# Kernel tuning notes

Hardware: AMD Instinct MI355X
Metric: run time of the kernel (lower is better)

## Reference

```python
import jax, jax.numpy as jnp
import numpy as np

HEADS = 4
KD = 32          # key_dim per head
LEVELS = 2
G = 3            # 2**dims - 1 HP orientation groups
STRENGTH = 0.25
DECAY = 0.6
LN_EPS = 1e-5
MIX_EPS = 1e-3


def _layernorm(x, g, b):
    m = jnp.mean(x, axis=-1, keepdims=True)
    v = jnp.var(x, axis=-1, keepdims=True)
    return (x - m) * jax.lax.rsqrt(v + LN_EPS) * g + b


def _dwt2(x):
    # Haar analysis, periodic/even sizes. [B,H,W,C] -> [B,H/2,W/2,4C] (LL,LH,HL,HH)
    x00 = x[:, 0::2, 0::2]; x01 = x[:, 0::2, 1::2]
    x10 = x[:, 1::2, 0::2]; x11 = x[:, 1::2, 1::2]
    ll = (x00 + x01 + x10 + x11) * 0.5
    lh = (x00 - x01 + x10 - x11) * 0.5
    hl = (x00 + x01 - x10 - x11) * 0.5
    hh = (x00 - x01 - x10 + x11) * 0.5
    return jnp.concatenate([ll, lh, hl, hh], axis=-1)


def _idwt2(w):
    # exact Haar synthesis: [B,H/2,W/2,4C] -> [B,H,W,C]
    ll, lh, hl, hh = jnp.split(w, 4, axis=-1)
    x00 = (ll + lh + hl + hh) * 0.5
    x01 = (ll - lh + hl - hh) * 0.5
    x10 = (ll + lh - hl - hh) * 0.5
    x11 = (ll - lh - hl + hh) * 0.5
    B, H2, W2, C = ll.shape
    r0 = jnp.stack([x00, x01], axis=3).reshape(B, H2, 2 * W2, C)  # interleave W
    r1 = jnp.stack([x10, x11], axis=3).reshape(B, H2, 2 * W2, C)
    return jnp.stack([r0, r1], axis=2).reshape(B, 2 * H2, 2 * W2, C)  # interleave H


def _axial_mhsa(x, p):
    # AxialMHSAND: sequential sweep over spatial axes; each pass is
    # proj(attn(softmax(QK^T/sqrt(d)) V)) on norm(x), qkv via 1x1 conv (=matmul).
    g, b, wq, bq, wk, bk, wv, bv, wp, bp = p
    scale = KD ** -0.5
    for axis in (1, 2):
        X = _layernorm(x, g, b)
        B, H, W, _ = X.shape
        Q = (X @ wq + bq).reshape(B, H, W, HEADS, KD)
        K = (X @ wk + bk).reshape(B, H, W, HEADS, KD)
        V = (X @ wv + bv).reshape(B, H, W, HEADS, KD)
        if axis == 1:  # attend along H, batch over (B, W, heads)
            A = jax.nn.softmax(jnp.einsum('bqwnd,bkwnd->bwnqk', Q, K) * scale, axis=-1)
            Y = jnp.einsum('bwnqk,bkwnd->bqwnd', A, V)
        else:          # attend along W, batch over (B, H, heads)
            A = jax.nn.softmax(jnp.einsum('bhqnd,bhknd->bhnqk', Q, K) * scale, axis=-1)
            Y = jnp.einsum('bhnqk,bhknd->bhqnd', A, V)
        x = Y.reshape(B, H, W, HEADS * KD) @ wp + bp
    return x


def setup_inputs() -> dict:
    key = jax.random.key(0)
    ks = jax.random.split(key, 24)
    C = 64
    HD = HEADS * KD
    s = 0.02
    inp = {'x': jax.random.normal(ks[0], (4, 256, 256, C), jnp.float32)}
    i = 1
    for pre in ('lp', 'hp'):
        inp[pre + '_ln_g'] = jnp.ones((C,), jnp.float32)
        inp[pre + '_ln_b'] = jnp.zeros((C,), jnp.float32)
        inp[pre + '_wq'] = jax.random.normal(ks[i], (C, HD), jnp.float32) * s
        inp[pre + '_bq'] = jax.random.normal(ks[i + 1], (HD,), jnp.float32) * s
        inp[pre + '_wk'] = jax.random.normal(ks[i + 2], (C, HD), jnp.float32) * s
        inp[pre + '_bk'] = jax.random.normal(ks[i + 3], (HD,), jnp.float32) * s
        inp[pre + '_wv'] = jax.random.normal(ks[i + 4], (C, HD), jnp.float32) * s
        inp[pre + '_bv'] = jax.random.normal(ks[i + 5], (HD,), jnp.float32) * s
        inp[pre + '_wp'] = jax.random.normal(ks[i + 6], (HD, C), jnp.float32) * s
        inp[pre + '_bp'] = jax.random.normal(ks[i + 7], (C,), jnp.float32) * s
        i += 8
    mix = jnp.eye(G, dtype=jnp.float32) + MIX_EPS * (jnp.ones((G, G), jnp.float32) - jnp.eye(G, dtype=jnp.float32))
    inp['mix_w0'] = mix
    inp['mix_w1'] = mix
    return inp


def reference(x, lp_ln_g, lp_ln_b, lp_wq, lp_bq, lp_wk, lp_bk, lp_wv, lp_bv, lp_wp, lp_bp,
              hp_ln_g, hp_ln_b, hp_wq, hp_bq, hp_wk, hp_bk, hp_wv, hp_bv, hp_wp, hp_bp,
              mix_w0, mix_w1):
    lp_p = (lp_ln_g, lp_ln_b, lp_wq, lp_bq, lp_wk, lp_bk, lp_wv, lp_bv, lp_wp, lp_bp)
    hp_p = (hp_ln_g, hp_ln_b, hp_wq, hp_bq, hp_wk, hp_bk, hp_wv, hp_bv, hp_wp, hp_bp)
    mix_ws = [mix_w0, mix_w1]
    C = x.shape[-1]
    cur = x
    hps = []
    for _ in range(LEVELS):  # analysis pyramid
        w = _dwt2(cur)
        hps.append(w[..., C:])
        cur = w[..., :C]
    # deepest LP: axial attention, residual with full strength
    cur = cur + STRENGTH * _axial_mhsa(cur, lp_p)
    for l in reversed(range(LEVELS)):  # synthesis with per-level HP processing
        hp = hps[l]
        B, H2, W2, _ = hp.shape
        gain = STRENGTH * (DECAY ** (LEVELS - 1 - l))  # coarser levels stronger
        hp_g = hp.reshape(B, H2, W2, G, C)
        mixed = jnp.einsum('gd,bhwdc->bhwgc', mix_ws[l], hp_g)  # OrientationMix
        batched = mixed.transpose(3, 0, 1, 2, 4).reshape(G * B, H2, W2, C)
        att = _axial_mhsa(batched, hp_p)  # shared hp_attn across groups/levels
        att = att.reshape(G, B, H2, W2, C).transpose(1, 2, 3, 0, 4).reshape(B, H2, W2, G * C)
        hp_out = hp + gain * att
        cur = _idwt2(jnp.concatenate([cur, hp_out], axis=-1))
    return cur
```

## Files before the change

kernel.cpp:

```cpp
#include <hip/hip_runtime.h>

#define LN_EPS 1e-5f
#define QSCALE 0.25500526578425445f

typedef __attribute__((ext_vector_type(8))) short bf16x8;
typedef __attribute__((ext_vector_type(4))) float f32x4;

#define MFMA16(A, B, C) __builtin_amdgcn_mfma_f32_16x16x32_bf16(A, B, C, 0, 0, 0)

static __device__ __forceinline__ unsigned short f2bf_rne(float f) {
    union { unsigned int i; float f; } c; c.f = f;
    unsigned int i = c.i;
    return (unsigned short)((i + 0x7fffu + ((i >> 16) & 1u)) >> 16);
}
static __device__ __forceinline__ void bfstore2(unsigned short* p, float x, float y) {
    *(unsigned int*)p = (unsigned int)f2bf_rne(x) | ((unsigned int)f2bf_rne(y) << 16);
}
static __device__ __forceinline__ unsigned pk2(float a, float b) {
    return __builtin_amdgcn_perm(__builtin_bit_cast(unsigned, b),
                                 __builtin_bit_cast(unsigned, a), 0x07060302u);
}
static __device__ __forceinline__ unsigned short tb16(float f) {
    return (unsigned short)(__builtin_bit_cast(unsigned, f) >> 16);
}
static __device__ __forceinline__ float bftrunc(float f) {
    return __builtin_bit_cast(float, __builtin_bit_cast(unsigned, f) & 0xFFFF0000u);
}

__global__ void dwt_kernel(const float4* __restrict__ in, float4* __restrict__ ll,
                           float4* __restrict__ hp, int B, int H2, int W2) {
    const int i = blockIdx.x * blockDim.x + threadIdx.x;
    const int total = B * H2 * W2 * 16;
    if (i >= total) return;
    const int c4 = i & 15;
    int t = i >> 4;
    const int w2 = t % W2; t /= W2;
    const int h2 = t % H2;
    const int b = t / H2;
    const int W = W2 * 2;
    const size_t base = (((size_t)b * (H2 * 2) + 2 * h2) * W + 2 * w2) * 16 + c4;
    const float4 x00 = in[base];
    const float4 x01 = in[base + 16];
    const float4 x10 = in[base + (size_t)W * 16];
    const float4 x11 = in[base + (size_t)W * 16 + 16];
    float4 vll, vlh, vhl, vhh;
#define DWTC(a) \
    vll.a = (x00.a + x01.a + x10.a + x11.a) * 0.5f; \
    vlh.a = (x00.a - x01.a + x10.a - x11.a) * 0.5f; \
    vhl.a = (x00.a + x01.a - x10.a - x11.a) * 0.5f; \
    vhh.a = (x00.a - x01.a - x10.a + x11.a) * 0.5f;
    DWTC(x) DWTC(y) DWTC(z) DWTC(w)
#undef DWTC
    const size_t oi = ((size_t)b * H2 + h2) * W2 + w2;
    ll[oi * 16 + c4] = vll;
    hp[oi * 48 + c4] = vlh;
    hp[oi * 48 + 16 + c4] = vhl;
    hp[oi * 48 + 32 + c4] = vhh;
}

__global__ void idwt_kernel(const float4* __restrict__ cur, const float4* __restrict__ hp,
                            const float4* __restrict__ att, float gain,
                            float4* __restrict__ out, int B, int H2, int W2) {
    const int i = blockIdx.x * blockDim.x + threadIdx.x;
    const int total = B * H2 * W2 * 16;
    if (i >= total) return;
    const int c4 = i & 15;
    int t = i >> 4;
    const int w2 = t % W2; t /= W2;
    const int h2 = t % H2;
    const int b = t / H2;
    const size_t oi = ((size_t)b * H2 + h2) * W2 + w2;
    const size_t sp = (size_t)h2 * W2 + w2;
    const size_t gstr = (size_t)B * H2 * W2;
    const float4 vll = cur[oi * 16 + c4];
    float4 vlh = hp[oi * 48 + c4];
    float4 vhl = hp[oi * 48 + 16 + c4];
    float4 vhh = hp[oi * 48 + 32 + c4];
    const float4 a0 = att[((size_t)b * H2 * W2 + sp) * 16 + c4];
    const float4 a1 = att[((size_t)b * H2 * W2 + gstr + sp) * 16 + c4];
    const float4 a2 = att[((size_t)b * H2 * W2 + 2 * gstr + sp) * 16 + c4];
#define ADDG(a) \
    vlh.a = fmaf(gain, a0.a, vlh.a); \
    vhl.a = fmaf(gain, a1.a, vhl.a); \
    vhh.a = fmaf(gain, a2.a, vhh.a);
    ADDG(x) ADDG(y) ADDG(z) ADDG(w)
#undef ADDG
    float4 x00, x01, x10, x11;
#define IDWTC(a) \
    x00.a = (vll.a + vlh.a + vhl.a + vhh.a) * 0.5f; \
    x01.a = (vll.a - vlh.a + vhl.a - vhh.a) * 0.5f; \
    x10.a = (vll.a + vlh.a - vhl.a - vhh.a) * 0.5f; \
    x11.a = (vll.a - vlh.a - vhl.a + vhh.a) * 0.5f;
    IDWTC(x) IDWTC(y) IDWTC(z) IDWTC(w)
#undef IDWTC
    const int W = W2 * 2;
    const size_t r0 = (((size_t)b * (H2 * 2) + 2 * h2) * W + 2 * w2) * 16 + c4;
    out[r0] = x00;
    out[r0 + 16] = x01;
    out[r0 + (size_t)W * 16] = x10;
    out[r0 + (size_t)W * 16 + 16] = x11;
}

__global__ void prep_weights(const float* __restrict__ lwq, const float* __restrict__ lwk,
                             const float* __restrict__ lwv, const float* __restrict__ lwp,
                             const float* __restrict__ hwq, const float* __restrict__ hwk,
                             const float* __restrict__ hwv, const float* __restrict__ hwp,
                             unsigned short* __restrict__ wbuf) {
    const int i = blockIdx.x * blockDim.x + threadIdx.x;
    if (i >= 65536) return;
    const int set = i >> 15;
    const int r = i & 32767;
    const float* wq = set ? hwq : lwq;
    const float* wk = set ? hwk : lwk;
    const float* wv = set ? hwv : lwv;
    const float* wp = set ? hwp : lwp;
    float v;
    if (r < 24576) {
        const int nn = r >> 6, c = r & 63;
        const float* w = (nn < 128) ? wq : (nn < 256) ? wk : wv;
        v = w[c * 128 + (nn & 127)];
        if (nn < 128) v *= QSCALE;
    } else {
        const int r2 = r - 24576;
        const int nn = r2 >> 7, d = r2 & 127;
        v = wp[d * 64 + nn];
    }
    wbuf[i] = f2bf_rne(v);
}

struct Job {
    const float* xin;
    const float* mixsrc;
    const float* mixw;
    float* xout;
    const float* basep;
    float res_scale;
    const float* ln_g; const float* ln_b;
    const float* bq; const float* bk; const float* bv; const float* bp;
    const unsigned short* wqkvT;
    const unsigned short* wpT;
};

template<int S>
__global__ __launch_bounds__(512, 4)
void axial_attn(Job jA, Job jB, int nA, int axis)
{
    constexpr int BS = 512;
    constexpr int CK = 32;
    constexpr int NCH = S / CK;
    constexpr int NSI = S / 32;
    constexpr int CSTR = 40;

    __shared__ __align__(16) unsigned short Xs[S * 64];
    __shared__ __align__(16) unsigned short Arena[18432];

    const int tid = threadIdx.x;
    const int lane = tid & 63;
    const int w = tid >> 6;
    const int n16 = lane & 15;
    const int quad = lane >> 4;

    const bool isB = (int)blockIdx.x >= nA;
    const Job j = isB ? jB : jA;
    const int line = isB ? (int)blockIdx.x - nA : (int)blockIdx.x;
    const int lb = line / S;
    const int lr = line - lb * S;
    size_t lbase, tstr;
    if (axis == 1) { lbase = ((size_t)lb * S * S + lr) * 64; tstr = (size_t)S * 64; }
    else           { lbase = ((size_t)lb * S + lr) * (size_t)S * 64; tstr = 64; }

    const float bk = j.bk[w * 16 + n16];
    const float bv = j.bv[w * 16 + n16];

    {
        const int sub = tid & 15;
        const float4 g4 = ((const float4*)j.ln_g)[sub];
        const float4 be4 = ((const float4*)j.ln_b)[sub];
        const float4* x4 = (const float4*)j.xin;
        const float4* hp4 = (const float4*)j.mixsrc;
        const size_t lbase4 = lbase >> 2, tstr4 = tstr >> 2;
        float m0, m1, m2; int bimg;
        if (hp4) {
            const int g = lb >> 2;
            bimg = lb & 3;
            m0 = j.mixw[g * 3 + 0]; m1 = j.mixw[g * 3 + 1]; m2 = j.mixw[g * 3 + 2];
        }
        for (int t = (tid >> 4); t < S; t += BS / 16) {
            float4 v;
            if (hp4) {
                const int pos = (axis == 1) ? (t * S + lr) : (lr * S + t);
                const size_t hb = ((size_t)bimg * S * S + pos) * 48 + sub;
                const float4 h0 = hp4[hb];
                const float4 h1 = hp4[hb + 16];
                const float4 h2 = hp4[hb + 32];
                v.x = m0 * h0.x + m1 * h1.x + m2 * h2.x;
                v.y = m0 * h0.y + m1 * h1.y + m2 * h2.y;
                v.z = m0 * h0.z + m1 * h1.z + m2 * h2.z;
                v.w = m0 * h0.w + m1 * h1.w + m2 * h2.w;
            } else {
                v = x4[lbase4 + (size_t)t * tstr4 + sub];
            }
            float s = v.x + v.y + v.z + v.w;
            float ss = v.x * v.x + v.y * v.y + v.z * v.z + v.w * v.w;
            #pragma unroll
            for (int m = 1; m < 16; m <<= 1) {
                s += __shfl_xor(s, m);
                ss += __shfl_xor(ss, m);
            }
            const float mean = s * 0.015625f;
            const float rstd = rsqrtf(ss * 0.015625f - mean * mean + LN_EPS);
            unsigned short* xr = &Xs[(t << 6) + ((sub * 4) ^ ((t & 7) << 3))];
            bfstore2(xr,     (v.x - mean) * rstd * g4.x + be4.x,
                             (v.y - mean) * rstd * g4.y + be4.y);
            bfstore2(xr + 2, (v.z - mean) * rstd * g4.z + be4.z,
                             (v.w - mean) * rstd * g4.w + be4.w);
        }
    }
    __syncthreads();

    {
        const float bias = j.bq[w * 16 + n16] * QSCALE;
        const bf16x8 Bq0 = *(const bf16x8*)&j.wqkvT[(w * 16 + n16) * 64 + quad * 8];
        const bf16x8 Bq1 = *(const bf16x8*)&j.wqkvT[(w * 16 + n16) * 64 + 32 + quad * 8];
        #pragma unroll
        for (int mt = 0; mt < S / 16; ++mt) {
            const int xr = mt * 16 + n16;
            const int xm = (xr & 7) << 3;
            const bf16x8 A0 = *(const bf16x8*)&Xs[(xr << 6) + ((quad * 8) ^ xm)];
            const bf16x8 A1 = *(const bf16x8*)&Xs[(xr << 6) + ((32 + quad * 8) ^ xm)];
            f32x4 acc = {bias, bias, bias, bias};
            acc = MFMA16(A0, Bq0, acc);
            acc = MFMA16(A1, Bq1, acc);
            const int row0 = mt * 16 + quad * 4;
            #pragma unroll
            for (int r = 0; r < 4; ++r) {
                const int rr = row0 + r;
                Arena[(rr << 7) + ((w * 16 + n16) ^ ((rr & 7) << 3))] = tb16(acc[r]);
            }
        }
    }
    __syncthreads();

    const int h = w >> 1;
    const int sub = w & 1;
    const int hoff = h * 32;

    bf16x8 qb[NSI];
    #pragma unroll
    for (int si = 0; si < NSI; ++si) {
        const int qr = (sub * NSI + si) * 16 + n16;
        qb[si] = *(const bf16x8*)&Arena[(qr << 7) + ((hoff + quad * 8) ^ ((qr & 7) << 3))];
    }
    f32x4 y0[NSI], y1[NSI];
    float rsum[NSI];
    #pragma unroll
    for (int si = 0; si < NSI; ++si) {
        y0[si] = (f32x4){0.f, 0.f, 0.f, 0.f};
        y1[si] = (f32x4){0.f, 0.f, 0.f, 0.f};
        rsum[si] = 0.f;
    }
    __syncthreads();

    auto produce = [&](int kc, int buf) {
        const int k0 = kc * CK;
        unsigned short* Kc = &Arena[buf * 4096];
        unsigned short* Vc = &Arena[8192 + buf * 5120];
        const bf16x8 Wk0 = *(const bf16x8*)&j.wqkvT[((8 + w) * 16 + n16) * 64 + quad * 8];
        const bf16x8 Wk1 = *(const bf16x8*)&j.wqkvT[((8 + w) * 16 + n16) * 64 + 32 + quad * 8];
        const bf16x8 Wv0 = *(const bf16x8*)&j.wqkvT[((16 + w) * 16 + n16) * 64 + quad * 8];
        const bf16x8 Wv1 = *(const bf16x8*)&j.wqkvT[((16 + w) * 16 + n16) * 64 + 32 + quad * 8];
        #pragma unroll
        for (int mtl = 0; mtl < 2; ++mtl) {
            const int xr = k0 + mtl * 16 + n16;
            const int xm = (xr & 7) << 3;
            const bf16x8 A0 = *(const bf16x8*)&Xs[(xr << 6) + ((quad * 8) ^ xm)];
            const bf16x8 A1 = *(const bf16x8*)&Xs[(xr << 6) + ((32 + quad * 8) ^ xm)];
            f32x4 ak = {bk, bk, bk, bk};
            ak = MFMA16(A0, Wk0, ak);
            ak = MFMA16(A1, Wk1, ak);
            const int row0 = mtl * 16 + quad * 4;
            #pragma unroll
            for (int r = 0; r < 4; ++r) {
                const int rr = row0 + r;
                Kc[(rr << 7) + ((w * 16 + n16) ^ ((rr & 7) << 3))] = tb16(ak[r]);
            }
            f32x4 av = {bv, bv, bv, bv};
            av = MFMA16(A0, Wv0, av);
            av = MFMA16(A1, Wv1, av);
            *(uint2*)&Vc[(w * 16 + n16) * CSTR + mtl * 16 + quad * 4] =
                make_uint2(pk2(av[0], av[1]), pk2(av[2], av[3]));
        }
    };

    const int sr0 = ((n16 >> 2) << 3) + (n16 & 3);
    const int sr1 = sr0 + 4;

    produce(0, 0);
    __syncthreads();
    for (int kc = 0; kc < NCH; ++kc) {
        const int buf = kc & 1;
        if (kc + 1 < NCH) produce(kc + 1, buf ^ 1);
        const unsigned short* Kc = &Arena[buf * 4096];
        const unsigned short* Vc = &Arena[8192 + buf * 5120];
        const bf16x8 ka0 = *(const bf16x8*)&Kc[(sr0 << 7) + ((hoff + quad * 8) ^ ((sr0 & 7) << 3))];
        const bf16x8 ka1 = *(const bf16x8*)&Kc[(sr1 << 7) + ((hoff + quad * 8) ^ ((sr1 & 7) << 3))];
        const bf16x8 vb0 = *(const bf16x8*)&Vc[(hoff + n16) * CSTR + quad * 8];
        const bf16x8 vb1 = *(const bf16x8*)&Vc[(hoff + 16 + n16) * CSTR + quad * 8];
        #pragma unroll
        for (int si = 0; si < NSI; ++si) {
            f32x4 sc0 = {0.f, 0.f, 0.f, 0.f};
            f32x4 sc1 = {0.f, 0.f, 0.f, 0.f};
            sc0 = MFMA16(ka0, qb[si], sc0);
            sc1 = MFMA16(ka1, qb[si], sc1);
            const float e0 = __builtin_amdgcn_exp2f(sc0[0]);
            const float e1 = __builtin_amdgcn_exp2f(sc0[1]);
            const float e2 = __builtin_amdgcn_exp2f(sc0[2]);
            const float e3 = __builtin_amdgcn_exp2f(sc0[3]);
            const float e4 = __builtin_amdgcn_exp2f(sc1[0]);
            const float e5 = __builtin_amdgcn_exp2f(sc1[1]);
            const float e6 = __builtin_amdgcn_exp2f(sc1[2]);
            const float e7 = __builtin_amdgcn_exp2f(sc1[3]);
            rsum[si] += ((bftrunc(e0) + bftrunc(e1)) + (bftrunc(e2) + bftrunc(e3)))
                      + ((bftrunc(e4) + bftrunc(e5)) + (bftrunc(e6) + bftrunc(e7)));
            union { unsigned u[4]; bf16x8 v; } pau;
            pau.u[0] = pk2(e0, e1);
            pau.u[1] = pk2(e2, e3);
            pau.u[2] = pk2(e4, e5);
            pau.u[3] = pk2(e6, e7);
            y0[si] = MFMA16(pau.v, vb0, y0[si]);
            y1[si] = MFMA16(pau.v, vb1, y1[si]);
        }
        __syncthreads();
    }

    #pragma unroll
    for (int si = 0; si < NSI; ++si) {
        float red = rsum[si];
        red += __shfl_xor(red, 16);
        red += __shfl_xor(red, 32);
        const int q0 = (sub * NSI + si) * 16;
        #pragma unroll
        for (int r = 0; r < 4; ++r) {
            const float inv = __builtin_amdgcn_rcpf(__shfl(red, quad * 4 + r));
            const int row = q0 + quad * 4 + r;
            const int m = (row & 7) << 3;
            Arena[(row << 7) + ((hoff + n16) ^ m)]      = tb16(y0[si][r] * inv);
            Arena[(row << 7) + ((hoff + 16 + n16) ^ m)] = tb16(y1[si][r] * inv);
        }
    }
    __syncthreads();

    {
        constexpr int TD = (S / 16) * 4 / 8;
        const int mt = (w * TD) >> 2;
        const int nt0 = (w * TD) & 3;
        const int m0 = mt * 16;
        const int ym = (n16 & 7) << 3;
        bf16x8 pa[4];
        #pragma unroll
        for (int kt = 0; kt < 4; ++kt)
            pa[kt] = *(const bf16x8*)&Arena[((m0 + n16) << 7) + ((kt * 32 + quad * 8) ^ ym)];
        #pragma unroll
        for (int i = 0; i < TD; ++i) {
            const int nt = nt0 + i;
            const float bias = j.bp[nt * 16 + n16];
            f32x4 acc = {bias, bias, bias, bias};
            #pragma unroll
            for (int kt = 0; kt < 4; ++kt) {
                const bf16x8 wb = *(const bf16x8*)&j.wpT[(nt * 16 + n16) * 128 + kt * 32 + quad * 8];
                acc = MFMA16(pa[kt], wb, acc);
            }
            #pragma unroll
            for (int r = 0; r < 4; ++r) {
                const size_t gi = lbase + (size_t)(m0 + quad * 4 + r) * tstr + nt * 16 + n16;
                float v = acc[r];
                if (j.basep) v = fmaf(j.res_scale, v, j.basep[gi]);
                j.xout[gi] = v;
            }
        }
    }
}

extern "C" void kernel_launch(void* const* d_in, const int* in_sizes, int n_in,
                              void* d_out, int out_size, void* d_ws, size_t ws_size,
                              hipStream_t stream) {
    (void)in_sizes; (void)n_in; (void)out_size; (void)ws_size;
    const float* x = (const float*)d_in[0];
    const float* P_lp[10];
    const float* P_hp[10];
    for (int i = 0; i < 10; ++i) P_lp[i] = (const float*)d_in[1 + i];
    for (int i = 0; i < 10; ++i) P_hp[i] = (const float*)d_in[11 + i];
    const float* mw0 = (const float*)d_in[21];
    const float* mw1 = (const float*)d_in[22];
    float* out = (float*)d_out;
    float* ws = (float*)d_ws;

    float* ll0 = ws;
    float* hp0 = ll0 + (size_t)4194304;
    float* t0  = hp0 + (size_t)12582912;
    float* ll1  = t0;
    float* hp1  = t0 + (size_t)1048576;
    float* ta2  = t0 + (size_t)4194304;
    float* lpta = t0 + (size_t)7340032;
    float* tb  = out;
    float* t1b = out;
    unsigned short* wbuf = (unsigned short*)(out + (size_t)13631488);

    prep_weights<<<256, 256, 0, stream>>>(
        P_lp[2], P_lp[4], P_lp[6], P_lp[8],
        P_hp[2], P_hp[4], P_hp[6], P_hp[8], wbuf);

    dwt_kernel<<<4 * 128 * 128 * 16 / 256, 256, 0, stream>>>(
        (const float4*)x, (float4*)ll0, (float4*)hp0, 4, 128, 128);
    dwt_kernel<<<4 * 64 * 64 * 16 / 256, 256, 0, stream>>>(
        (const float4*)ll0, (float4*)ll1, (float4*)hp1, 4, 64, 64);

    const unsigned short* lp_qkvT = wbuf;
    const unsigned short* lp_wpT  = wbuf + 24576;
    const unsigned short* hp_qkvT = wbuf + 32768;
    const unsigned short* hp_wpT  = wbuf + 32768 + 24576;

    auto mkjob = [](const float* xin, const float* mixsrc, const float* mixw,
                    float* xout, const float* basep, float rs,
                    const float* const* P, const unsigned short* qkvT,
                    const unsigned short* wpT) {
        Job jj;
        jj.xin = xin; jj.mixsrc = mixsrc; jj.mixw = mixw;
        jj.xout = xout; jj.basep = basep; jj.res_scale = rs;
        jj.ln_g = P[0]; jj.ln_b = P[1];
        jj.bq = P[3]; jj.bk = P[5]; jj.bv = P[7]; jj.bp = P[9];
        jj.wqkvT = qkvT; jj.wpT = wpT;
        return jj;
    };

    {
        Job a1 = mkjob(ll1, nullptr, nullptr, lpta, nullptr, 1.f, P_lp, lp_qkvT, lp_wpT);
        Job b1 = mkjob(nullptr, hp1, mw1, tb, nullptr, 1.f, P_hp, hp_qkvT, hp_wpT);
        axial_attn<64><<<1024, 512, 0, stream>>>(a1, b1, 256, 1);
        Job a2 = mkjob(lpta, nullptr, nullptr, ll1, ll1, 0.25f, P_lp, lp_qkvT, lp_wpT);
        Job b2 = mkjob(tb, nullptr, nullptr, ta2, nullptr, 1.f, P_hp, hp_qkvT, hp_wpT);
        axial_attn<64><<<1024, 512, 0, stream>>>(a2, b2, 256, 2);
    }
    idwt_kernel<<<4 * 64 * 64 * 16 / 256, 256, 0, stream>>>(
        (const float4*)ll1, (const float4*)hp1, (const float4*)ta2, 0.25f,
        (float4*)ll0, 4, 64, 64);

    {
        Job c1 = mkjob(nullptr, hp0, mw0, t1b, nullptr, 1.f, P_hp, hp_qkvT, hp_wpT);
        axial_attn<128><<<1536, 512, 0, stream>>>(c1, c1, 1536, 1);
        Job c2 = mkjob(t1b, nullptr, nullptr, t0, nullptr, 1.f, P_hp, hp_qkvT, hp_wpT);
        axial_attn<128><<<1536, 512, 0, stream>>>(c2, c2, 1536, 2);
    }
    idwt_kernel<<<4 * 128 * 128 * 16 / 256, 256, 0, stream>>>(
        (const float4*)ll0, (const float4*)hp0, (const float4*)t0, 0.15f,
        (float4*)out, 4, 128, 128);
}
```

Before: 409.5 us.

## Split each attention line across two blocks by query half

Each axial line is now handled by two blocks, each owning half of the query rows. Both blocks still recompute LayerNorm over the full line and rebuild K/V for all keys. The Arena layout is reorganised to interleave K/V buffers and move the Q stash to an offset, and the launch bound rises to 6 blocks per CU. K/V weight loads are hoisted out of the produce lambda, one barrier is removed, and the MFMA/exp ordering in the softmax loop is tweaked. The aim is more parallelism and occupancy, at the cost of duplicated LN and K/V projection work plus higher register pressure.

```diff
diff --git a/kernel.cpp b/kernel.cpp
--- a/kernel.cpp
+++ b/kernel.cpp
@@ -142,13 +142,13 @@
 };
 
 template<int S>
-__global__ __launch_bounds__(512, 4)
-void axial_attn(Job jA, Job jB, int nA, int axis)
+__global__ __launch_bounds__(512, 6)
+void axial_attn(Job jA, Job jB, int nAlines, int nlines, int axis)
 {
-    constexpr int BS = 512;
     constexpr int CK = 32;
     constexpr int NCH = S / CK;
-    constexpr int NSI = S / 32;
+    constexpr int HS = S / 2;
+    constexpr int NSI = HS / 32;
     constexpr int CSTR = 40;
 
     __shared__ __align__(16) unsigned short Xs[S * 64];
@@ -160,15 +160,21 @@
     const int n16 = lane & 15;
     const int quad = lane >> 4;
 
-    const bool isB = (int)blockIdx.x >= nA;
+    const int qhalf = (int)blockIdx.x / nlines;
+    const int lg = (int)blockIdx.x - qhalf * nlines;
+    const bool isB = lg >= nAlines;
     const Job j = isB ? jB : jA;
-    const int line = isB ? (int)blockIdx.x - nA : (int)blockIdx.x;
+    const int line = isB ? lg - nAlines : lg;
     const int lb = line / S;
     const int lr = line - lb * S;
     size_t lbase, tstr;
     if (axis == 1) { lbase = ((size_t)lb * S * S + lr) * 64; tstr = (size_t)S * 64; }
     else           { lbase = ((size_t)lb * S + lr) * (size_t)S * 64; tstr = 64; }
 
+    const bf16x8 Wk0 = *(const bf16x8*)&j.wqkvT[((8 + w) * 16 + n16) * 64 + quad * 8];
+    const bf16x8 Wk1 = *(const bf16x8*)&j.wqkvT[((8 + w) * 16 + n16) * 64 + 32 + quad * 8];
+    const bf16x8 Wv0 = *(const bf16x8*)&j.wqkvT[((16 + w) * 16 + n16) * 64 + quad * 8];
+    const bf16x8 Wv1 = *(const bf16x8*)&j.wqkvT[((16 + w) * 16 + n16) * 64 + 32 + quad * 8];
     const float bk = j.bk[w * 16 + n16];
     const float bv = j.bv[w * 16 + n16];
 
@@ -185,7 +191,7 @@
             bimg = lb & 3;
             m0 = j.mixw[g * 3 + 0]; m1 = j.mixw[g * 3 + 1]; m2 = j.mixw[g * 3 + 2];
         }
-        for (int t = (tid >> 4); t < S; t += BS / 16) {
+        for (int t = (tid >> 4); t < S; t += 32) {
             float4 v;
             if (hp4) {
                 const int pos = (axis == 1) ? (t * S + lr) : (lr * S + t);
@@ -223,8 +229,8 @@
         const bf16x8 Bq0 = *(const bf16x8*)&j.wqkvT[(w * 16 + n16) * 64 + quad * 8];
         const bf16x8 Bq1 = *(const bf16x8*)&j.wqkvT[(w * 16 + n16) * 64 + 32 + quad * 8];
         #pragma unroll
-        for (int mt = 0; mt < S / 16; ++mt) {
-            const int xr = mt * 16 + n16;
+        for (int mt = 0; mt < HS / 16; ++mt) {
+            const int xr = qhalf * HS + mt * 16 + n16;
             const int xm = (xr & 7) << 3;
             const bf16x8 A0 = *(const bf16x8*)&Xs[(xr << 6) + ((quad * 8) ^ xm)];
             const bf16x8 A1 = *(const bf16x8*)&Xs[(xr << 6) + ((32 + quad * 8) ^ xm)];
@@ -235,7 +241,7 @@
             #pragma unroll
             for (int r = 0; r < 4; ++r) {
                 const int rr = row0 + r;
-                Arena[(rr << 7) + ((w * 16 + n16) ^ ((rr & 7) << 3))] = tb16(acc[r]);
+                Arena[9216 + (rr << 7) + ((w * 16 + n16) ^ ((rr & 7) << 3))] = tb16(acc[r]);
             }
         }
     }
@@ -249,7 +255,7 @@
     #pragma unroll
     for (int si = 0; si < NSI; ++si) {
         const int qr = (sub * NSI + si) * 16 + n16;
-        qb[si] = *(const bf16x8*)&Arena[(qr << 7) + ((hoff + quad * 8) ^ ((qr & 7) << 3))];
+        qb[si] = *(const bf16x8*)&Arena[9216 + (qr << 7) + ((hoff + quad * 8) ^ ((qr & 7) << 3))];
     }
     f32x4 y0[NSI], y1[NSI];
     float rsum[NSI];
@@ -259,16 +265,11 @@
         y1[si] = (f32x4){0.f, 0.f, 0.f, 0.f};
         rsum[si] = 0.f;
     }
-    __syncthreads();
 
     auto produce = [&](int kc, int buf) {
         const int k0 = kc * CK;
-        unsigned short* Kc = &Arena[buf * 4096];
-        unsigned short* Vc = &Arena[8192 + buf * 5120];
-        const bf16x8 Wk0 = *(const bf16x8*)&j.wqkvT[((8 + w) * 16 + n16) * 64 + quad * 8];
-        const bf16x8 Wk1 = *(const bf16x8*)&j.wqkvT[((8 + w) * 16 + n16) * 64 + 32 + quad * 8];
-        const bf16x8 Wv0 = *(const bf16x8*)&j.wqkvT[((16 + w) * 16 + n16) * 64 + quad * 8];
-        const bf16x8 Wv1 = *(const bf16x8*)&j.wqkvT[((16 + w) * 16 + n16) * 64 + 32 + quad * 8];
+        unsigned short* Kc = &Arena[buf * 9216];
+        unsigned short* Vc = &Arena[buf * 9216 + 4096];
         #pragma unroll
         for (int mtl = 0; mtl < 2; ++mtl) {
             const int xr = k0 + mtl * 16 + n16;
@@ -300,8 +301,8 @@
     for (int kc = 0; kc < NCH; ++kc) {
         const int buf = kc & 1;
         if (kc + 1 < NCH) produce(kc + 1, buf ^ 1);
-        const unsigned short* Kc = &Arena[buf * 4096];
-        const unsigned short* Vc = &Arena[8192 + buf * 5120];
+        const unsigned short* Kc = &Arena[buf * 9216];
+        const unsigned short* Vc = &Arena[buf * 9216 + 4096];
         const bf16x8 ka0 = *(const bf16x8*)&Kc[(sr0 << 7) + ((hoff + quad * 8) ^ ((sr0 & 7) << 3))];
         const bf16x8 ka1 = *(const bf16x8*)&Kc[(sr1 << 7) + ((hoff + quad * 8) ^ ((sr1 & 7) << 3))];
         const bf16x8 vb0 = *(const bf16x8*)&Vc[(hoff + n16) * CSTR + quad * 8];
@@ -309,19 +310,17 @@
         #pragma unroll
         for (int si = 0; si < NSI; ++si) {
             f32x4 sc0 = {0.f, 0.f, 0.f, 0.f};
-            f32x4 sc1 = {0.f, 0.f, 0.f, 0.f};
             sc0 = MFMA16(ka0, qb[si], sc0);
-            sc1 = MFMA16(ka1, qb[si], sc1);
             const float e0 = __builtin_amdgcn_exp2f(sc0[0]);
             const float e1 = __builtin_amdgcn_exp2f(sc0[1]);
             const float e2 = __builtin_amdgcn_exp2f(sc0[2]);
             const float e3 = __builtin_amdgcn_exp2f(sc0[3]);
+            f32x4 sc1 = {0.f, 0.f, 0.f, 0.f};
+            sc1 = MFMA16(ka1, qb[si], sc1);
             const float e4 = __builtin_amdgcn_exp2f(sc1[0]);
             const float e5 = __builtin_amdgcn_exp2f(sc1[1]);
             const float e6 = __builtin_amdgcn_exp2f(sc1[2]);
             const float e7 = __builtin_amdgcn_exp2f(sc1[3]);
-            rsum[si] += ((bftrunc(e0) + bftrunc(e1)) + (bftrunc(e2) + bftrunc(e3)))
-                      + ((bftrunc(e4) + bftrunc(e5)) + (bftrunc(e6) + bftrunc(e7)));
             union { unsigned u[4]; bf16x8 v; } pau;
             pau.u[0] = pk2(e0, e1);
             pau.u[1] = pk2(e2, e3);
@@ -329,6 +328,8 @@
             pau.u[3] = pk2(e6, e7);
             y0[si] = MFMA16(pau.v, vb0, y0[si]);
             y1[si] = MFMA16(pau.v, vb1, y1[si]);
+            rsum[si] += ((bftrunc(e0) + bftrunc(e1)) + (bftrunc(e2) + bftrunc(e3)))
+                      + ((bftrunc(e4) + bftrunc(e5)) + (bftrunc(e6) + bftrunc(e7)));
         }
         __syncthreads();
     }
@@ -351,7 +352,7 @@
     __syncthreads();
 
     {
-        constexpr int TD = (S / 16) * 4 / 8;
+        constexpr int TD = (HS / 16) * 4 / 8;
         const int mt = (w * TD) >> 2;
         const int nt0 = (w * TD) & 3;
         const int m0 = mt * 16;
@@ -372,7 +373,7 @@
             }
             #pragma unroll
             for (int r = 0; r < 4; ++r) {
-                const size_t gi = lbase + (size_t)(m0 + quad * 4 + r) * tstr + nt * 16 + n16;
+                const size_t gi = lbase + (size_t)(qhalf * HS + m0 + quad * 4 + r) * tstr + nt * 16 + n16;
                 float v = acc[r];
                 if (j.basep) v = fmaf(j.res_scale, v, j.basep[gi]);
                 j.xout[gi] = v;
@@ -436,10 +437,10 @@
     {
         Job a1 = mkjob(ll1, nullptr, nullptr, lpta, nullptr, 1.f, P_lp, lp_qkvT, lp_wpT);
         Job b1 = mkjob(nullptr, hp1, mw1, tb, nullptr, 1.f, P_hp, hp_qkvT, hp_wpT);
-        axial_attn<64><<<1024, 512, 0, stream>>>(a1, b1, 256, 1);
+        axial_attn<64><<<2048, 512, 0, stream>>>(a1, b1, 256, 1024, 1);
         Job a2 = mkjob(lpta, nullptr, nullptr, ll1, ll1, 0.25f, P_lp, lp_qkvT, lp_wpT);
         Job b2 = mkjob(tb, nullptr, nullptr, ta2, nullptr, 1.f, P_hp, hp_qkvT, hp_wpT);
-        axial_attn<64><<<1024, 512, 0, stream>>>(a2, b2, 256, 2);
+        axial_attn<64><<<2048, 512, 0, stream>>>(a2, b2, 256, 1024, 2);
     }
     idwt_kernel<<<4 * 64 * 64 * 16 / 256, 256, 0, stream>>>(
         (const float4*)ll1, (const float4*)hp1, (const float4*)ta2, 0.25f,
@@ -447,9 +448,9 @@
 
     {
         Job c1 = mkjob(nullptr, hp0, mw0, t1b, nullptr, 1.f, P_hp, hp_qkvT, hp_wpT);
-        axial_attn<128><<<1536, 512, 0, stream>>>(c1, c1, 1536, 1);
+        axial_attn<128><<<3072, 512, 0, stream>>>(c1, c1, 1536, 1536, 1);
         Job c2 = mkjob(t1b, nullptr, nullptr, t0, nullptr, 1.f, P_hp, hp_qkvT, hp_wpT);
-        axial_attn<128><<<1536, 512, 0, stream>>>(c2, c2, 1536, 2);
+        axial_attn<128><<<3072, 512, 0, stream>>>(c2, c2, 1536, 1536, 2);
     }
     idwt_kernel<<<4 * 128 * 128 * 16 / 256, 256, 0, stream>>>(
         (const float4*)ll0, (const float4*)hp0, (const float4*)t0, 0.15f,
```

New measurement: 526.0 us. +28.5%, slower.
